# Kernel optimization log

Hardware: AMD Instinct MI355X
Metric: run time of the kernel (lower is better)

## Reference

```python
import jax, jax.numpy as jnp
import numpy as np

N_HEAD = 16


def setup_inputs() -> dict:
    key = jax.random.key(0)
    ks = jax.random.split(key, 5)
    B, T, C = 4, 2048, 1024
    s = 0.02
    x = jax.random.normal(ks[0], (B, T, C), jnp.float32)
    wq = jax.random.normal(ks[1], (C, C), jnp.float32) * s
    wk = jax.random.normal(ks[2], (C, C), jnp.float32) * s
    wv = jax.random.normal(ks[3], (C, C), jnp.float32) * s
    wp = jax.random.normal(ks[4], (C, C), jnp.float32) * s
    zb = jnp.zeros((C,), jnp.float32)
    return {"x": x, "wq": wq, "bq": zb, "wk": wk, "bk": zb,
            "wv": wv, "bv": zb, "wp": wp, "bp": zb}


def _rope_cos_sin(T, D):
    half = D // 2
    i = jnp.arange(half, dtype=jnp.float32)
    alpha = 1.0 / (10000.0 ** (2.0 * i / D))        # [half]
    ang = jnp.arange(T, dtype=jnp.float32)[:, None] * alpha  # [T, half]
    return jnp.cos(ang), jnp.sin(ang)


def _apply_rope(t, cos, sin):
    # t: [B, H, T, D]; non-interleaved halves as in the torch module
    half = t.shape[-1] // 2
    xr, xi = t[..., :half], t[..., half:]
    return jnp.concatenate([xr * cos - xi * sin, xr * sin + xi * cos], axis=-1)


def reference(x, wq, bq, wk, bk, wv, bv, wp, bp):
    B, T, C = x.shape
    H = N_HEAD
    D = C // H
    # QKV projections (torch Linear: x @ W.T + b)
    def heads(w, b):
        return (x @ w.T + b).reshape(B, T, H, D).transpose(0, 2, 1, 3)
    q, k, v = heads(wq, bq), heads(wk, bk), heads(wv, bv)
    cos, sin = _rope_cos_sin(T, D)  # each [T, D//2], broadcasts over B,H
    q = _apply_rope(q, cos, sin)
    k = _apply_rope(k, cos, sin)
    scale = 1.0 / np.sqrt(D).astype(np.float32)
    att = jnp.einsum('bhtd,bhsd->bhts', q, k) * scale  # [B,H,T,T]
    causal = jnp.tril(jnp.ones((T, T), bool))
    att = jnp.where(causal, att, jnp.float32(-jnp.inf))
    att = jax.nn.softmax(att, axis=-1)
    y = jnp.einsum('bhts,bhsd->bhtd', att, v)  # [B,H,T,D]
    y = y.transpose(0, 2, 1, 3).reshape(B, T, C)
    return y @ wp.T + bp
```

## Files before the change

### kernel.cpp

```cpp
#include <hip/hip_runtime.h>
#include <math.h>

constexpr int B = 4, T = 2048, C = 1024, H = 16, D = 64;
constexpr int M = B * T;
constexpr size_t BTC = (size_t)B * T * C;
constexpr float QSCALE = 0.18033688011112042f;
constexpr float ROPE_C = -0.415241011861f;

typedef short bf16x8 __attribute__((ext_vector_type(8)));
typedef float f32x4 __attribute__((ext_vector_type(4)));

__device__ inline ushort f2bf(float f) {
  union { float f; unsigned u; } cv; cv.f = f;
  unsigned u = cv.u;
  u += 0x7fffu + ((u >> 16) & 1u);
  return (ushort)(u >> 16);
}
__device__ inline ushort f2bfr(float f) {
  union { float f; unsigned u; } cv; cv.f = f;
  return (ushort)((cv.u + 0x8000u) >> 16);
}

__device__ inline void async_load16(const void* g, void* l) {
  __builtin_amdgcn_global_load_lds(
      (const __attribute__((address_space(1))) void*)g,
      (__attribute__((address_space(3))) void*)l, 16, 0, 0);
}

__device__ __forceinline__ bf16x8 ones_frag() {
  bf16x8 v;
#pragma unroll
  for (int i = 0; i < 8; i++) v[i] = (short)0x3F80;
  return v;
}

__global__ __launch_bounds__(256) void f32_to_bf16(
    const float* __restrict__ in, ushort* __restrict__ outp) {
  int i = (blockIdx.x * 256 + threadIdx.x) * 4;
  float4 v = *(const float4*)(in + i);
  ushort4 o;
  o.x = f2bf(v.x); o.y = f2bf(v.y); o.z = f2bf(v.z); o.w = f2bf(v.w);
  *(ushort4*)(outp + i) = o;
}

__global__ __launch_bounds__(256) void conv_weights(
    const float* __restrict__ w0, const float* __restrict__ w1,
    const float* __restrict__ w2, const float* __restrict__ w3,
    ushort* __restrict__ outp) {
  const int seg_blocks = (C * C) / 1024;
  int seg = blockIdx.x / seg_blocks;
  int blk = blockIdx.x - seg * seg_blocks;
  const float* src = (seg == 0) ? w0 : (seg == 1) ? w1 : (seg == 2) ? w2 : w3;
  int i = (blk * 256 + threadIdx.x) * 4;
  float4 v = *(const float4*)(src + i);
  ushort4 o;
  o.x = f2bf(v.x); o.y = f2bf(v.y); o.z = f2bf(v.z); o.w = f2bf(v.w);
  *(ushort4*)(outp + (size_t)seg * C * C + i) = o;
}

#define GT 128
#define GBK 64
template <int OM>
__global__ __launch_bounds__(256) void gemm_mfma_bt(
    const ushort* __restrict__ A, const ushort* __restrict__ Wt,
    const float* __restrict__ b0, const float* __restrict__ b1,
    const float* __restrict__ b2, void* __restrict__ out1,
    void* __restrict__ out2, void* __restrict__ out3,
    int N, int K) {
  __shared__ ushort As[GT * GBK] __attribute__((aligned(16)));
  __shared__ ushort Bs[GT * GBK] __attribute__((aligned(16)));
  int tid = threadIdx.x;
  int lane = tid & 63;
  int lrow = lane & 15, quad = lane >> 4;
  int wave = tid >> 6;
  int wr = wave >> 1, wc = wave & 1;
  int row0 = blockIdx.y * GT;
  int col0 = blockIdx.x * GT;
  const float* bias = (col0 < 1024) ? b0 : (col0 < 2048) ? b1 : b2;

  size_t ga[4], gb[4];
#pragma unroll
  for (int i = 0; i < 4; i++) {
    int cc = tid + i * 256;
    int r = cc >> 3, cl = cc & 7;
    int g = (cl ^ (r & 7)) * 8;
    ga[i] = (size_t)(row0 + r) * K + g;
    gb[i] = (size_t)(col0 + r) * K + g;
  }
  int x7 = lrow & 7;

  f32x4 acc[4][4];
#pragma unroll
  for (int i = 0; i < 4; i++)
#pragma unroll
    for (int j = 0; j < 4; j++) acc[i][j] = (f32x4){0.f, 0.f, 0.f, 0.f};

  for (int k0 = 0; k0 < K; k0 += GBK) {
#pragma unroll
    for (int i = 0; i < 4; i++) {
      int cc = tid + i * 256;
      async_load16(A + ga[i] + k0, &As[cc * 8]);
      async_load16(Wt + gb[i] + k0, &Bs[cc * 8]);
    }
    __syncthreads();
#pragma unroll
    for (int kh = 0; kh < 2; kh++) {
      int slot = ((kh * 4 + quad) ^ x7) * 8;
      bf16x8 af[4], bfr[4];
#pragma unroll
      for (int i = 0; i < 4; i++)
        af[i] = *(const bf16x8*)&As[(wr * 64 + i * 16 + lrow) * GBK + slot];
#pragma unroll
      for (int j = 0; j < 4; j++)
        bfr[j] = *(const bf16x8*)&Bs[(wc * 64 + j * 16 + lrow) * GBK + slot];
#pragma unroll
      for (int i = 0; i < 4; i++)
#pragma unroll
        for (int j = 0; j < 4; j++)
          acc[i][j] = __builtin_amdgcn_mfma_f32_16x16x32_bf16(af[i], bfr[j], acc[i][j], 0, 0, 0);
    }
    __syncthreads();
  }

  int nb = col0 + wc * 64;
  int mbase = row0 + wr * 64;
  float bn[4];
#pragma unroll
  for (int j = 0; j < 4; j++) bn[j] = bias[(nb & 1023) + j * 16 + lrow];

  if (OM == 0) {
    float* outp = (float*)out1;
#pragma unroll
    for (int i = 0; i < 4; i++)
#pragma unroll
      for (int j = 0; j < 4; j++) {
        int n = nb + j * 16 + lrow;
#pragma unroll
        for (int r = 0; r < 4; r++) {
          int m = mbase + i * 16 + quad * 4 + r;
          outp[(size_t)m * N + n] = acc[i][j][r] + bn[j];
        }
      }
  } else {
    int seg = nb >> 10;
    int hh = (nb & 1023) >> 6;
    if (seg < 2) {
      ushort* dst = (seg == 0) ? (ushort*)out1 : (ushort*)out2;
      float scale = (seg == 0) ? QSCALE : 1.0f;
      float a0 = __builtin_amdgcn_exp2f((float)lrow * ROPE_C);
      float a1 = __builtin_amdgcn_exp2f((float)(lrow + 16) * ROPE_C);
#pragma unroll
      for (int i = 0; i < 4; i++) {
#pragma unroll
        for (int r = 0; r < 4; r++) {
          int m = mbase + i * 16 + quad * 4 + r;
          int t = m & (T - 1), bb = m >> 11;
          float s0, c0, s1, c1;
          __sincosf((float)t * a0, &s0, &c0);
          __sincosf((float)t * a1, &s1, &c1);
          float xr0 = acc[i][0][r] + bn[0];
          float xi0 = acc[i][2][r] + bn[2];
          float xr1 = acc[i][1][r] + bn[1];
          float xi1 = acc[i][3][r] + bn[3];
          ushort* p = dst + ((size_t)(bb * H + hh) * T + t) * D + lrow;
          p[0]  = f2bf((xr0 * c0 - xi0 * s0) * scale);
          p[32] = f2bf((xr0 * s0 + xi0 * c0) * scale);
          p[16] = f2bf((xr1 * c1 - xi1 * s1) * scale);
          p[48] = f2bf((xr1 * s1 + xi1 * c1) * scale);
        }
      }
    } else {
      ushort* dst = (ushort*)out3;
#pragma unroll
      for (int i = 0; i < 4; i++) {
        int m0 = mbase + i * 16 + quad * 4;
        int t0 = m0 & (T - 1), bb = m0 >> 11;
        size_t base = (size_t)(bb * H + hh) * D * T + t0;
#pragma unroll
        for (int j = 0; j < 4; j++) {
          int d = j * 16 + lrow;
          ushort4 pk;
          pk.x = f2bf(acc[i][j][0] + bn[j]);
          pk.y = f2bf(acc[i][j][1] + bn[j]);
          pk.z = f2bf(acc[i][j][2] + bn[j]);
          pk.w = f2bf(acc[i][j][3] + bn[j]);
          *(ushort4*)(dst + base + (size_t)d * T) = pk;
        }
      }
    }
  }
}

__device__ __forceinline__ void stage_kv(
    const ushort* kbh, const ushort* vbh, int s0,
    ushort* Kl, ushort* Vl, int tid) {
#pragma unroll
  for (int i = 0; i < 2; i++) {
    int c = tid + i * 256;
    int r = c >> 3, cc = c & 7;
    int g = (cc ^ (r & 7)) * 8;
    async_load16(kbh + (size_t)(s0 + r) * D + g, Kl + c * 8);
    async_load16(vbh + (size_t)r * T + s0 + g, Vl + c * 8);
  }
}

template <int MODE>
__device__ __forceinline__ void attn_step4(
    int s0, const ushort* KL, const ushort* VL, ushort* P,
    const bf16x8 (&qf)[2][2], int lrow, int quad, int sw0, int sw1,
    int qg0, int qg1, f32x4 (&o)[4][2], f32x4 (&ol)[2]) {
  bf16x8 kf0[4], kf1[4];
#pragma unroll
  for (int kt = 0; kt < 4; kt++) {
    int base = (kt * 16 + lrow) * 64;
    kf0[kt] = *(const bf16x8*)&KL[base + sw0];
    kf1[kt] = *(const bf16x8*)&KL[base + sw1];
  }
  bf16x8 vf0[4], vf1[4];
#pragma unroll
  for (int ds = 0; ds < 4; ds++) {
    int base = (ds * 16 + lrow) * 64;
    vf0[ds] = *(const bf16x8*)&VL[base + sw0];
    vf1[ds] = *(const bf16x8*)&VL[base + sw1];
  }
#pragma unroll
  for (int g = 0; g < 2; g++) {
    if (MODE == 2 && g == 0) continue;
    int qg = g ? qg1 : qg0;
    f32x4 st[4];
#pragma unroll
    for (int kt = 0; kt < 4; kt++) {
      f32x4 z = {0.f, 0.f, 0.f, 0.f};
      st[kt] = __builtin_amdgcn_mfma_f32_16x16x32_bf16(kf0[kt], qf[g][0], z, 0, 0, 0);
      st[kt] = __builtin_amdgcn_mfma_f32_16x16x32_bf16(kf1[kt], qf[g][1], st[kt], 0, 0, 0);
    }
    if ((MODE == 1 && g == 0) || (MODE == 2 && g == 1)) {
#pragma unroll
      for (int kt = 0; kt < 4; kt++)
#pragma unroll
        for (int r = 0; r < 4; r++)
          if (s0 + kt * 16 + quad * 4 + r > qg) st[kt][r] = -1e30f;
    }
#pragma unroll
    for (int kt = 0; kt < 4; kt++) {
      ushort4 pk;
      pk.x = f2bfr(__builtin_amdgcn_exp2f(st[kt][0]));
      pk.y = f2bfr(__builtin_amdgcn_exp2f(st[kt][1]));
      pk.z = f2bfr(__builtin_amdgcn_exp2f(st[kt][2]));
      pk.w = f2bfr(__builtin_amdgcn_exp2f(st[kt][3]));
      *(ushort4*)&P[((2 * kt + (quad >> 1)) * 32 + g * 16 + lrow) * 8 + (quad & 1) * 4] = pk;
    }
  }
  asm volatile("" ::: "memory");
  bf16x8 ones = ones_frag();
#pragma unroll
  for (int g = 0; g < 2; g++) {
    if (MODE == 2 && g == 0) continue;
    bf16x8 pf0 = *(const bf16x8*)&P[(quad * 32 + g * 16 + lrow) * 8];
    bf16x8 pf1 = *(const bf16x8*)&P[((quad + 4) * 32 + g * 16 + lrow) * 8];
    ol[g] = __builtin_amdgcn_mfma_f32_16x16x32_bf16(ones, pf0, ol[g], 0, 0, 0);
    ol[g] = __builtin_amdgcn_mfma_f32_16x16x32_bf16(ones, pf1, ol[g], 0, 0, 0);
#pragma unroll
    for (int ds = 0; ds < 4; ds++) {
      o[ds][g] = __builtin_amdgcn_mfma_f32_16x16x32_bf16(vf0[ds], pf0, o[ds][g], 0, 0, 0);
      o[ds][g] = __builtin_amdgcn_mfma_f32_16x16x32_bf16(vf1[ds], pf1, o[ds][g], 0, 0, 0);
    }
  }
}

__global__ __launch_bounds__(256, 3) void attn_mfma4(
    const ushort* __restrict__ qb_, const ushort* __restrict__ kb_,
    const ushort* __restrict__ vtb_, ushort* __restrict__ y) {
  __shared__ ushort Kl[2][64 * 64] __attribute__((aligned(16)));
  __shared__ ushort Vl[2][64 * 64] __attribute__((aligned(16)));
  __shared__ ushort Pl[4][2048] __attribute__((aligned(16)));
  int tid = threadIdx.x;
  int wave = tid >> 6, lane = tid & 63;
  int lrow = lane & 15, quad = lane >> 4;
  int qbi = 15 - (int)(blockIdx.x >> 6);
  int bh = blockIdx.x & 63;
  int b = bh >> 4, h = bh & 15;
  int Q0 = qbi * 128;
  ushort* P = Pl[wave];
  const ushort* kbh = kb_ + (size_t)bh * T * D;
  const ushort* vbh = vtb_ + (size_t)bh * D * T;

  int qg0 = Q0 + wave * 16 + lrow;
  int qg1 = qg0 + 64;
  bf16x8 qf[2][2];
  {
    const ushort* qp0 = qb_ + ((size_t)bh * T + qg0) * D + quad * 8;
    qf[0][0] = *(const bf16x8*)qp0;
    qf[0][1] = *(const bf16x8*)(qp0 + 32);
    const ushort* qp1 = qb_ + ((size_t)bh * T + qg1) * D + quad * 8;
    qf[1][0] = *(const bf16x8*)qp1;
    qf[1][1] = *(const bf16x8*)(qp1 + 32);
  }
  int r7 = lrow & 7;
  int sw0 = (quad ^ r7) * 8;
  int sw1 = ((quad + 4) ^ r7) * 8;

  f32x4 o[4][2];
#pragma unroll
  for (int ds = 0; ds < 4; ds++)
#pragma unroll
    for (int g = 0; g < 2; g++) o[ds][g] = (f32x4){0.f, 0.f, 0.f, 0.f};
  f32x4 ol[2] = {(f32x4){0.f, 0.f, 0.f, 0.f}, (f32x4){0.f, 0.f, 0.f, 0.f}};

  int trips = 2 * qbi + 2;
  stage_kv(kbh, vbh, 0, Kl[0], Vl[0], tid);
  int it = 0;
  for (; it < trips - 2; ++it) {
    __syncthreads();
    stage_kv(kbh, vbh, (it + 1) * 64, Kl[(it + 1) & 1], Vl[(it + 1) & 1], tid);
    attn_step4<0>(it * 64, Kl[it & 1], Vl[it & 1], P, qf, lrow, quad, sw0, sw1,
                  qg0, qg1, o, ol);
  }
  __syncthreads();
  stage_kv(kbh, vbh, (it + 1) * 64, Kl[(it + 1) & 1], Vl[(it + 1) & 1], tid);
  attn_step4<1>(it * 64, Kl[it & 1], Vl[it & 1], P, qf, lrow, quad, sw0, sw1,
                qg0, qg1, o, ol);
  ++it;
  __syncthreads();
  attn_step4<2>(it * 64, Kl[it & 1], Vl[it & 1], P, qf, lrow, quad, sw0, sw1,
                qg0, qg1, o, ol);

#pragma unroll
  for (int g = 0; g < 2; g++) {
    float inv = 1.f / ol[g][0];
    int qg = g ? qg1 : qg0;
#pragma unroll
    for (int ds = 0; ds < 4; ds++) {
      ushort4 pk;
      pk.x = f2bf(o[ds][g][0] * inv);
      pk.y = f2bf(o[ds][g][1] * inv);
      pk.z = f2bf(o[ds][g][2] * inv);
      pk.w = f2bf(o[ds][g][3] * inv);
      *(ushort4*)(y + ((size_t)b * T + qg) * C + h * D + ds * 16 + quad * 4) = pk;
    }
  }
}

extern "C" void kernel_launch(void* const* d_in, const int* in_sizes, int n_in,
                              void* d_out, int out_size, void* d_ws, size_t ws_size,
                              hipStream_t stream) {
  const float* x  = (const float*)d_in[0];
  const float* wq = (const float*)d_in[1];
  const float* bq = (const float*)d_in[2];
  const float* wk = (const float*)d_in[3];
  const float* bk = (const float*)d_in[4];
  const float* wv = (const float*)d_in[5];
  const float* bv = (const float*)d_in[6];
  const float* wp = (const float*)d_in[7];
  const float* bp = (const float*)d_in[8];
  float* out = (float*)d_out;

  ushort* xb    = (ushort*)d_ws;
  ushort* qb    = xb + BTC;
  ushort* kb    = qb + BTC;
  ushort* vtb   = kb + BTC;
  ushort* yb    = vtb + BTC;
  ushort* wqkvb = yb + BTC;
  ushort* wpb   = wqkvb + (size_t)3 * C * C;

  f32_to_bf16<<<(int)(BTC / 1024), 256, 0, stream>>>(x, xb);
  conv_weights<<<4 * (C * C) / 1024, 256, 0, stream>>>(wq, wk, wv, wp, wqkvb);

  dim3 qkv_grid(3 * C / GT, M / GT);
  gemm_mfma_bt<1><<<qkv_grid, 256, 0, stream>>>(
      xb, wqkvb, bq, bk, bv, qb, kb, vtb, 3 * C, C);

  attn_mfma4<<<(B * H * T / 128), 256, 0, stream>>>(qb, kb, vtb, yb);

  dim3 proj_grid(C / GT, M / GT);
  gemm_mfma_bt<0><<<proj_grid, 256, 0, stream>>>(
      yb, wpb, bp, bp, bp, out, nullptr, nullptr, C, C);
}
```

Baseline: 246.8 us.

## Replace QKV GEMM with 256x256 double-buffered 8-wave MFMA kernel

Adds a dedicated QKV projection kernel that uses 256x256 output tiles with 512 threads. A/B tiles are double-buffered in LDS through async global-to-LDS loads, the MFMA phases are split into four quadrants interleaved with barriers and s_setprio, and block indices are swizzled for L2 locality. The RoPE/scale/V-transpose epilogue moves into the new kernel and is removed from the generic GEMM template. The goal is more operand reuse per LDS byte and load latency hidden behind compute, at the cost of heavy register and LDS use (128KB shared) and fewer blocks in flight.

Result: slower. 252.4 us (+2.3%).

```diff
diff --git a/kernel.cpp b/kernel.cpp
--- a/kernel.cpp
+++ b/kernel.cpp
@@ -56,6 +56,217 @@
   ushort4 o;
   o.x = f2bf(v.x); o.y = f2bf(v.y); o.z = f2bf(v.z); o.w = f2bf(v.w);
   *(ushort4*)(outp + (size_t)seg * C * C + i) = o;
+}
+
+constexpr int QNT = C / 64;
+
+__global__ __launch_bounds__(512, 2) void gemm256_qkv(
+    const ushort* __restrict__ A, const ushort* __restrict__ Wt,
+    const float* __restrict__ b0, const float* __restrict__ b1,
+    const float* __restrict__ b2, ushort* __restrict__ outq,
+    ushort* __restrict__ outk, ushort* __restrict__ outv) {
+  __shared__ ushort As[2][256 * 64] __attribute__((aligned(16)));
+  __shared__ ushort Bs[2][256 * 64] __attribute__((aligned(16)));
+  const int tid = threadIdx.x;
+  const int lane = tid & 63;
+  const int lrow = lane & 15, quad = lane >> 4;
+  const int wave = tid >> 6;
+  const int wr = wave >> 2, wc = wave & 3;
+
+  int bid = blockIdx.y * 12 + blockIdx.x;
+  int lin = (bid & 7) * 48 + (bid >> 3);
+  int row0 = (lin / 12) * 256;
+  int col0 = (lin % 12) * 256;
+
+  unsigned ga[4], gb[4];
+#pragma unroll
+  for (int i = 0; i < 4; i++) {
+    int c = tid + i * 512;
+    int r = c >> 3, cl = c & 7;
+    int g = (cl ^ (r & 7)) * 8;
+    ga[i] = (unsigned)(row0 + r) * C + g;
+    gb[i] = (unsigned)(col0 + r) * C + g;
+  }
+
+  f32x4 acc[8][4];
+#pragma unroll
+  for (int i = 0; i < 8; i++)
+#pragma unroll
+    for (int j = 0; j < 4; j++) acc[i][j] = (f32x4){0.f, 0.f, 0.f, 0.f};
+
+  const int x7 = lrow & 7;
+  const int sl0 = ((0 * 4 + quad) ^ x7) * 8;
+  const int sl1 = ((1 * 4 + quad) ^ x7) * 8;
+
+#pragma unroll
+  for (int i = 0; i < 4; i++)
+    async_load16(A + ga[i], &As[0][(tid + i * 512) * 8]);
+#pragma unroll
+  for (int i = 0; i < 4; i++)
+    async_load16(Wt + gb[i], &Bs[0][(tid + i * 512) * 8]);
+#pragma unroll
+  for (int i = 0; i < 4; i++)
+    async_load16(A + ga[i] + 64, &As[1][(tid + i * 512) * 8]);
+  asm volatile("s_waitcnt vmcnt(4)" ::: "memory");
+  __builtin_amdgcn_sched_barrier(0);
+  __builtin_amdgcn_s_barrier();
+
+  for (int t = 0; t < QNT; ++t) {
+    const int p = t & 1;
+    const ushort* Ap = As[p];
+    const ushort* Bp = Bs[p];
+    ushort* Bnext = Bs[p ^ 1];
+
+    bf16x8 af[4][2], bf0[2][2];
+#pragma unroll
+    for (int mf = 0; mf < 4; mf++) {
+      const ushort* rp = &Ap[(wr * 128 + mf * 16 + lrow) * 64];
+      af[mf][0] = *(const bf16x8*)(rp + sl0);
+      af[mf][1] = *(const bf16x8*)(rp + sl1);
+    }
+#pragma unroll
+    for (int nf = 0; nf < 2; nf++) {
+      const ushort* rp = &Bp[(wc * 64 + nf * 16 + lrow) * 64];
+      bf0[nf][0] = *(const bf16x8*)(rp + sl0);
+      bf0[nf][1] = *(const bf16x8*)(rp + sl1);
+    }
+    if (t + 1 < QNT) {
+#pragma unroll
+      for (int i = 0; i < 4; i++)
+        async_load16(Wt + gb[i] + (t + 1) * 64, &Bnext[(tid + i * 512) * 8]);
+    }
+    __builtin_amdgcn_s_barrier();
+    __builtin_amdgcn_s_setprio(1);
+#pragma unroll
+    for (int mf = 0; mf < 4; mf++)
+#pragma unroll
+      for (int nf = 0; nf < 2; nf++) {
+        acc[mf][nf] = __builtin_amdgcn_mfma_f32_16x16x32_bf16(
+            af[mf][0], bf0[nf][0], acc[mf][nf], 0, 0, 0);
+        acc[mf][nf] = __builtin_amdgcn_mfma_f32_16x16x32_bf16(
+            af[mf][1], bf0[nf][1], acc[mf][nf], 0, 0, 0);
+      }
+    __builtin_amdgcn_s_setprio(0);
+    __builtin_amdgcn_s_barrier();
+
+    bf16x8 bf1[2][2];
+#pragma unroll
+    for (int nf = 0; nf < 2; nf++) {
+      const ushort* rp = &Bp[(wc * 64 + (2 + nf) * 16 + lrow) * 64];
+      bf1[nf][0] = *(const bf16x8*)(rp + sl0);
+      bf1[nf][1] = *(const bf16x8*)(rp + sl1);
+    }
+    __builtin_amdgcn_s_barrier();
+    __builtin_amdgcn_s_setprio(1);
+#pragma unroll
+    for (int mf = 0; mf < 4; mf++)
+#pragma unroll
+      for (int nf = 0; nf < 2; nf++) {
+        acc[mf][2 + nf] = __builtin_amdgcn_mfma_f32_16x16x32_bf16(
+            af[mf][0], bf1[nf][0], acc[mf][2 + nf], 0, 0, 0);
+        acc[mf][2 + nf] = __builtin_amdgcn_mfma_f32_16x16x32_bf16(
+            af[mf][1], bf1[nf][1], acc[mf][2 + nf], 0, 0, 0);
+      }
+    __builtin_amdgcn_s_setprio(0);
+    __builtin_amdgcn_s_barrier();
+
+    bf16x8 af2[4][2];
+#pragma unroll
+    for (int mf = 0; mf < 4; mf++) {
+      const ushort* rp = &Ap[(wr * 128 + 64 + mf * 16 + lrow) * 64];
+      af2[mf][0] = *(const bf16x8*)(rp + sl0);
+      af2[mf][1] = *(const bf16x8*)(rp + sl1);
+    }
+    __builtin_amdgcn_s_barrier();
+    __builtin_amdgcn_s_setprio(1);
+#pragma unroll
+    for (int mf = 0; mf < 4; mf++)
+#pragma unroll
+      for (int nf = 0; nf < 2; nf++) {
+        acc[4 + mf][2 + nf] = __builtin_amdgcn_mfma_f32_16x16x32_bf16(
+            af2[mf][0], bf1[nf][0], acc[4 + mf][2 + nf], 0, 0, 0);
+        acc[4 + mf][2 + nf] = __builtin_amdgcn_mfma_f32_16x16x32_bf16(
+            af2[mf][1], bf1[nf][1], acc[4 + mf][2 + nf], 0, 0, 0);
+      }
+    __builtin_amdgcn_s_setprio(0);
+    __builtin_amdgcn_s_barrier();
+
+    if (t + 2 < QNT) {
+#pragma unroll
+      for (int i = 0; i < 4; i++)
+        async_load16(A + ga[i] + (t + 2) * 64, &As[p][(tid + i * 512) * 8]);
+      asm volatile("s_waitcnt vmcnt(4)" ::: "memory");
+    } else {
+      asm volatile("s_waitcnt vmcnt(0)" ::: "memory");
+    }
+    __builtin_amdgcn_sched_barrier(0);
+    __builtin_amdgcn_s_barrier();
+    __builtin_amdgcn_s_setprio(1);
+#pragma unroll
+    for (int mf = 0; mf < 4; mf++)
+#pragma unroll
+      for (int nf = 0; nf < 2; nf++) {
+        acc[4 + mf][nf] = __builtin_amdgcn_mfma_f32_16x16x32_bf16(
+            af2[mf][0], bf0[nf][0], acc[4 + mf][nf], 0, 0, 0);
+        acc[4 + mf][nf] = __builtin_amdgcn_mfma_f32_16x16x32_bf16(
+            af2[mf][1], bf0[nf][1], acc[4 + mf][nf], 0, 0, 0);
+      }
+    __builtin_amdgcn_s_setprio(0);
+    __builtin_amdgcn_s_barrier();
+  }
+
+  const int nb = col0 + wc * 64;
+  const int mbase = row0 + wr * 128;
+  const float* bias = (col0 < 1024) ? b0 : (col0 < 2048) ? b1 : b2;
+  float bn[4];
+#pragma unroll
+  for (int j = 0; j < 4; j++) bn[j] = bias[(nb & 1023) + j * 16 + lrow];
+
+  int seg = nb >> 10;
+  int hh = (nb & 1023) >> 6;
+  if (seg < 2) {
+    ushort* dst = (seg == 0) ? outq : outk;
+    float scale = (seg == 0) ? QSCALE : 1.0f;
+    float a0 = __builtin_amdgcn_exp2f((float)lrow * ROPE_C);
+    float a1 = __builtin_amdgcn_exp2f((float)(lrow + 16) * ROPE_C);
+#pragma unroll
+    for (int mf = 0; mf < 8; mf++) {
+#pragma unroll
+      for (int r = 0; r < 4; r++) {
+        int m = mbase + mf * 16 + quad * 4 + r;
+        int tt = m & (T - 1), bb = m >> 11;
+        float s0, c0, s1, c1;
+        __sincosf((float)tt * a0, &s0, &c0);
+        __sincosf((float)tt * a1, &s1, &c1);
+        float xr0 = acc[mf][0][r] + bn[0];
+        float xi0 = acc[mf][2][r] + bn[2];
+        float xr1 = acc[mf][1][r] + bn[1];
+        float xi1 = acc[mf][3][r] + bn[3];
+        ushort* pp = dst + ((size_t)(bb * H + hh) * T + tt) * D + lrow;
+        pp[0]  = f2bf((xr0 * c0 - xi0 * s0) * scale);
+        pp[32] = f2bf((xr0 * s0 + xi0 * c0) * scale);
+        pp[16] = f2bf((xr1 * c1 - xi1 * s1) * scale);
+        pp[48] = f2bf((xr1 * s1 + xi1 * c1) * scale);
+      }
+    }
+  } else {
+#pragma unroll
+    for (int mf = 0; mf < 8; mf++) {
+      int m0 = mbase + mf * 16 + quad * 4;
+      int t0 = m0 & (T - 1), bb = m0 >> 11;
+      size_t base = (size_t)(bb * H + hh) * D * T + t0;
+#pragma unroll
+      for (int j = 0; j < 4; j++) {
+        int d = j * 16 + lrow;
+        ushort4 pk;
+        pk.x = f2bf(acc[mf][j][0] + bn[j]);
+        pk.y = f2bf(acc[mf][j][1] + bn[j]);
+        pk.z = f2bf(acc[mf][j][2] + bn[j]);
+        pk.w = f2bf(acc[mf][j][3] + bn[j]);
+        *(ushort4*)(outv + base + (size_t)d * T) = pk;
+      }
+    }
+  }
 }
 
 #define GT 128
@@ -141,53 +352,6 @@
           outp[(size_t)m * N + n] = acc[i][j][r] + bn[j];
         }
       }
-  } else {
-    int seg = nb >> 10;
-    int hh = (nb & 1023) >> 6;
-    if (seg < 2) {
-      ushort* dst = (seg == 0) ? (ushort*)out1 : (ushort*)out2;
-      float scale = (seg == 0) ? QSCALE : 1.0f;
-      float a0 = __builtin_amdgcn_exp2f((float)lrow * ROPE_C);
-      float a1 = __builtin_amdgcn_exp2f((float)(lrow + 16) * ROPE_C);
-#pragma unroll
-      for (int i = 0; i < 4; i++) {
-#pragma unroll
-        for (int r = 0; r < 4; r++) {
-          int m = mbase + i * 16 + quad * 4 + r;
-          int t = m & (T - 1), bb = m >> 11;
-          float s0, c0, s1, c1;
-          __sincosf((float)t * a0, &s0, &c0);
-          __sincosf((float)t * a1, &s1, &c1);
-          float xr0 = acc[i][0][r] + bn[0];
-          float xi0 = acc[i][2][r] + bn[2];
-          float xr1 = acc[i][1][r] + bn[1];
-          float xi1 = acc[i][3][r] + bn[3];
-          ushort* p = dst + ((size_t)(bb * H + hh) * T + t) * D + lrow;
-          p[0]  = f2bf((xr0 * c0 - xi0 * s0) * scale);
-          p[32] = f2bf((xr0 * s0 + xi0 * c0) * scale);
-          p[16] = f2bf((xr1 * c1 - xi1 * s1) * scale);
-          p[48] = f2bf((xr1 * s1 + xi1 * c1) * scale);
-        }
-      }
-    } else {
-      ushort* dst = (ushort*)out3;
-#pragma unroll
-      for (int i = 0; i < 4; i++) {
-        int m0 = mbase + i * 16 + quad * 4;
-        int t0 = m0 & (T - 1), bb = m0 >> 11;
-        size_t base = (size_t)(bb * H + hh) * D * T + t0;
-#pragma unroll
-        for (int j = 0; j < 4; j++) {
-          int d = j * 16 + lrow;
-          ushort4 pk;
-          pk.x = f2bf(acc[i][j][0] + bn[j]);
-          pk.y = f2bf(acc[i][j][1] + bn[j]);
-          pk.z = f2bf(acc[i][j][2] + bn[j]);
-          pk.w = f2bf(acc[i][j][3] + bn[j]);
-          *(ushort4*)(dst + base + (size_t)d * T) = pk;
-        }
-      }
-    }
   }
 }
 
@@ -366,9 +530,9 @@
   f32_to_bf16<<<(int)(BTC / 1024), 256, 0, stream>>>(x, xb);
   conv_weights<<<4 * (C * C) / 1024, 256, 0, stream>>>(wq, wk, wv, wp, wqkvb);
 
-  dim3 qkv_grid(3 * C / GT, M / GT);
-  gemm_mfma_bt<1><<<qkv_grid, 256, 0, stream>>>(
-      xb, wqkvb, bq, bk, bv, qb, kb, vtb, 3 * C, C);
+  dim3 qkv_grid(3 * C / 256, M / 256);
+  gemm256_qkv<<<qkv_grid, 512, 0, stream>>>(
+      xb, wqkvb, bq, bk, bv, qb, kb, vtb);
 
   attn_mfma4<<<(B * H * T / 128), 256, 0, stream>>>(qb, kb, vtb, yb);
 
```

## Add dedicated 256x128 QKV GEMM with async double-buffered pipelining and block swizzle

Applied to the files above, without the earlier changes.

Replaces the generic 128x128 QKV projection GEMM with a specialized 512-thread kernel using 256x128 tiles. A is double-buffered and B triple-buffered in LDS via async global-to-LDS loads issued one step ahead, with explicit waitcnt and barriers, s_setprio around the MFMA bursts, and a block-index remap for L2 locality. The aim is to overlap global loads with MFMA work and raise data reuse per tile. In exchange it uses much more LDS per block (about 112 KB), which limits occupancy, and it relies on hand-placed synchronization, where a mistake would corrupt results.

Result: no change. 247.2 us (+0.2%).

```diff
diff --git a/kernel.cpp b/kernel.cpp
--- a/kernel.cpp
+++ b/kernel.cpp
@@ -56,6 +56,187 @@
   ushort4 o;
   o.x = f2bf(v.x); o.y = f2bf(v.y); o.z = f2bf(v.z); o.w = f2bf(v.w);
   *(ushort4*)(outp + (size_t)seg * C * C + i) = o;
+}
+
+constexpr int QNT = C / 64;
+
+__global__ __launch_bounds__(512, 2) void gemm_qkv_256x128(
+    const ushort* __restrict__ A, const ushort* __restrict__ Wt,
+    const float* __restrict__ b0, const float* __restrict__ b1,
+    const float* __restrict__ b2, ushort* __restrict__ outq,
+    ushort* __restrict__ outk, ushort* __restrict__ outv) {
+  __shared__ ushort As[2][256 * 64] __attribute__((aligned(16)));
+  __shared__ ushort Bs[3][128 * 64] __attribute__((aligned(16)));
+  const int tid = threadIdx.x;
+  const int lane = tid & 63;
+  const int lrow = lane & 15, quad = lane >> 4;
+  const int wave = tid >> 6;
+  const int wr = wave >> 1, wc = wave & 1;
+  const int x7 = lrow & 7;
+
+  int bid = blockIdx.y * 24 + blockIdx.x;
+  int lin = (bid & 7) * 96 + (bid >> 3);
+  int row0 = (lin / 24) * 256;
+  int col0 = (lin % 24) * 128;
+
+  unsigned gaA[4], gaB[2];
+#pragma unroll
+  for (int i = 0; i < 4; i++) {
+    int c = tid + i * 512;
+    int r = c >> 3, cl = c & 7;
+    gaA[i] = (unsigned)(row0 + r) * C + (cl ^ (r & 7)) * 8;
+  }
+#pragma unroll
+  for (int i = 0; i < 2; i++) {
+    int c = tid + i * 512;
+    int r = c >> 3, cl = c & 7;
+    gaB[i] = (unsigned)(col0 + r) * C + (cl ^ (r & 7)) * 8;
+  }
+
+  f32x4 acc[4][4];
+#pragma unroll
+  for (int i = 0; i < 4; i++)
+#pragma unroll
+    for (int j = 0; j < 4; j++) acc[i][j] = (f32x4){0.f, 0.f, 0.f, 0.f};
+
+#pragma unroll
+  for (int i = 0; i < 4; i++)
+    async_load16(A + gaA[i], &As[0][(tid + i * 512) * 8]);
+#pragma unroll
+  for (int i = 0; i < 2; i++)
+    async_load16(Wt + gaB[i], &Bs[0][(tid + i * 512) * 8]);
+#pragma unroll
+  for (int i = 0; i < 2; i++)
+    async_load16(Wt + gaB[i] + 64, &Bs[1][(tid + i * 512) * 8]);
+  asm volatile("s_waitcnt vmcnt(2)" ::: "memory");
+  __builtin_amdgcn_sched_barrier(0);
+  __builtin_amdgcn_s_barrier();
+
+  int bi = 0;
+  for (int t = 0; t < QNT; ++t) {
+    const int pa = t & 1;
+    const ushort* Ap = As[pa];
+    const ushort* Bp = Bs[bi];
+
+    {
+      const int slot = (quad ^ x7) * 8;
+      bf16x8 af[4], bfr[4];
+#pragma unroll
+      for (int i = 0; i < 4; i++)
+        af[i] = *(const bf16x8*)&Ap[(wr * 64 + i * 16 + lrow) * 64 + slot];
+#pragma unroll
+      for (int j = 0; j < 4; j++)
+        bfr[j] = *(const bf16x8*)&Bp[(wc * 64 + j * 16 + lrow) * 64 + slot];
+      if (t + 1 < QNT) {
+#pragma unroll
+        for (int i = 0; i < 4; i++)
+          async_load16(A + gaA[i] + (t + 1) * 64,
+                       &As[pa ^ 1][(tid + i * 512) * 8]);
+      }
+      __builtin_amdgcn_s_barrier();
+      asm volatile("s_waitcnt lgkmcnt(0)" ::: "memory");
+      __builtin_amdgcn_sched_barrier(0);
+      __builtin_amdgcn_s_setprio(1);
+#pragma unroll
+      for (int i = 0; i < 4; i++)
+#pragma unroll
+        for (int j = 0; j < 4; j++)
+          acc[i][j] = __builtin_amdgcn_mfma_f32_16x16x32_bf16(
+              af[i], bfr[j], acc[i][j], 0, 0, 0);
+      __builtin_amdgcn_s_setprio(0);
+      __builtin_amdgcn_s_barrier();
+    }
+
+    {
+      const int slot = ((4 + quad) ^ x7) * 8;
+      bf16x8 af[4], bfr[4];
+#pragma unroll
+      for (int i = 0; i < 4; i++)
+        af[i] = *(const bf16x8*)&Ap[(wr * 64 + i * 16 + lrow) * 64 + slot];
+#pragma unroll
+      for (int j = 0; j < 4; j++)
+        bfr[j] = *(const bf16x8*)&Bp[(wc * 64 + j * 16 + lrow) * 64 + slot];
+      if (t + 2 < QNT) {
+        int bi2 = bi - 1; if (bi2 < 0) bi2 = 2;
+#pragma unroll
+        for (int i = 0; i < 2; i++)
+          async_load16(Wt + gaB[i] + (t + 2) * 64,
+                       &Bs[bi2][(tid + i * 512) * 8]);
+      }
+      __builtin_amdgcn_s_barrier();
+      asm volatile("s_waitcnt lgkmcnt(0)" ::: "memory");
+      __builtin_amdgcn_sched_barrier(0);
+      __builtin_amdgcn_s_setprio(1);
+#pragma unroll
+      for (int i = 0; i < 4; i++)
+#pragma unroll
+        for (int j = 0; j < 4; j++)
+          acc[i][j] = __builtin_amdgcn_mfma_f32_16x16x32_bf16(
+              af[i], bfr[j], acc[i][j], 0, 0, 0);
+      __builtin_amdgcn_s_setprio(0);
+      if (t + 2 < QNT) {
+        asm volatile("s_waitcnt vmcnt(2)" ::: "memory");
+      } else {
+        asm volatile("s_waitcnt vmcnt(0)" ::: "memory");
+      }
+      __builtin_amdgcn_sched_barrier(0);
+      __builtin_amdgcn_s_barrier();
+    }
+    bi = (bi + 1 == 3) ? 0 : bi + 1;
+  }
+
+  const int nb = col0 + wc * 64;
+  const int mbase = row0 + wr * 64;
+  const float* bias = (col0 < 1024) ? b0 : (col0 < 2048) ? b1 : b2;
+  float bn[4];
+#pragma unroll
+  for (int j = 0; j < 4; j++) bn[j] = bias[(nb & 1023) + j * 16 + lrow];
+
+  int seg = nb >> 10;
+  int hh = (nb & 1023) >> 6;
+  if (seg < 2) {
+    ushort* dst = (seg == 0) ? outq : outk;
+    float scale = (seg == 0) ? QSCALE : 1.0f;
+    float a0 = __builtin_amdgcn_exp2f((float)lrow * ROPE_C);
+    float a1 = __builtin_amdgcn_exp2f((float)(lrow + 16) * ROPE_C);
+#pragma unroll
+    for (int i = 0; i < 4; i++) {
+#pragma unroll
+      for (int r = 0; r < 4; r++) {
+        int m = mbase + i * 16 + quad * 4 + r;
+        int tt = m & (T - 1), bb = m >> 11;
+        float s0, c0, s1, c1;
+        __sincosf((float)tt * a0, &s0, &c0);
+        __sincosf((float)tt * a1, &s1, &c1);
+        float xr0 = acc[i][0][r] + bn[0];
+        float xi0 = acc[i][2][r] + bn[2];
+        float xr1 = acc[i][1][r] + bn[1];
+        float xi1 = acc[i][3][r] + bn[3];
+        ushort* pp = dst + ((size_t)(bb * H + hh) * T + tt) * D + lrow;
+        pp[0]  = f2bf((xr0 * c0 - xi0 * s0) * scale);
+        pp[32] = f2bf((xr0 * s0 + xi0 * c0) * scale);
+        pp[16] = f2bf((xr1 * c1 - xi1 * s1) * scale);
+        pp[48] = f2bf((xr1 * s1 + xi1 * c1) * scale);
+      }
+    }
+  } else {
+#pragma unroll
+    for (int i = 0; i < 4; i++) {
+      int m0 = mbase + i * 16 + quad * 4;
+      int t0 = m0 & (T - 1), bb = m0 >> 11;
+      size_t base = (size_t)(bb * H + hh) * D * T + t0;
+#pragma unroll
+      for (int j = 0; j < 4; j++) {
+        int d = j * 16 + lrow;
+        ushort4 pk;
+        pk.x = f2bf(acc[i][j][0] + bn[j]);
+        pk.y = f2bf(acc[i][j][1] + bn[j]);
+        pk.z = f2bf(acc[i][j][2] + bn[j]);
+        pk.w = f2bf(acc[i][j][3] + bn[j]);
+        *(ushort4*)(outv + base + (size_t)d * T) = pk;
+      }
+    }
+  }
 }
 
 #define GT 128
@@ -141,53 +322,6 @@
           outp[(size_t)m * N + n] = acc[i][j][r] + bn[j];
         }
       }
-  } else {
-    int seg = nb >> 10;
-    int hh = (nb & 1023) >> 6;
-    if (seg < 2) {
-      ushort* dst = (seg == 0) ? (ushort*)out1 : (ushort*)out2;
-      float scale = (seg == 0) ? QSCALE : 1.0f;
-      float a0 = __builtin_amdgcn_exp2f((float)lrow * ROPE_C);
-      float a1 = __builtin_amdgcn_exp2f((float)(lrow + 16) * ROPE_C);
-#pragma unroll
-      for (int i = 0; i < 4; i++) {
-#pragma unroll
-        for (int r = 0; r < 4; r++) {
-          int m = mbase + i * 16 + quad * 4 + r;
-          int t = m & (T - 1), bb = m >> 11;
-          float s0, c0, s1, c1;
-          __sincosf((float)t * a0, &s0, &c0);
-          __sincosf((float)t * a1, &s1, &c1);
-          float xr0 = acc[i][0][r] + bn[0];
-          float xi0 = acc[i][2][r] + bn[2];
-          float xr1 = acc[i][1][r] + bn[1];
-          float xi1 = acc[i][3][r] + bn[3];
-          ushort* p = dst + ((size_t)(bb * H + hh) * T + t) * D + lrow;
-          p[0]  = f2bf((xr0 * c0 - xi0 * s0) * scale);
-          p[32] = f2bf((xr0 * s0 + xi0 * c0) * scale);
-          p[16] = f2bf((xr1 * c1 - xi1 * s1) * scale);
-          p[48] = f2bf((xr1 * s1 + xi1 * c1) * scale);
-        }
-      }
-    } else {
-      ushort* dst = (ushort*)out3;
-#pragma unroll
-      for (int i = 0; i < 4; i++) {
-        int m0 = mbase + i * 16 + quad * 4;
-        int t0 = m0 & (T - 1), bb = m0 >> 11;
-        size_t base = (size_t)(bb * H + hh) * D * T + t0;
-#pragma unroll
-        for (int j = 0; j < 4; j++) {
-          int d = j * 16 + lrow;
-          ushort4 pk;
-          pk.x = f2bf(acc[i][j][0] + bn[j]);
-          pk.y = f2bf(acc[i][j][1] + bn[j]);
-          pk.z = f2bf(acc[i][j][2] + bn[j]);
-          pk.w = f2bf(acc[i][j][3] + bn[j]);
-          *(ushort4*)(dst + base + (size_t)d * T) = pk;
-        }
-      }
-    }
   }
 }
 
@@ -366,9 +500,9 @@
   f32_to_bf16<<<(int)(BTC / 1024), 256, 0, stream>>>(x, xb);
   conv_weights<<<4 * (C * C) / 1024, 256, 0, stream>>>(wq, wk, wv, wp, wqkvb);
 
-  dim3 qkv_grid(3 * C / GT, M / GT);
-  gemm_mfma_bt<1><<<qkv_grid, 256, 0, stream>>>(
-      xb, wqkvb, bq, bk, bv, qb, kb, vtb, 3 * C, C);
+  dim3 qkv_grid(3 * C / 128, M / 256);
+  gemm_qkv_256x128<<<qkv_grid, 512, 0, stream>>>(
+      xb, wqkvb, bq, bk, bv, qb, kb, vtb);
 
   attn_mfma4<<<(B * H * T / 128), 256, 0, stream>>>(qb, kb, vtb, yb);
 
```
